# Kernel tuning notes

Measured on AMD Instinct MI355X. Metric: run time of the kernel, lower is better.

Reference implementation:

```python
import jax, jax.numpy as jnp
import numpy as np

N = 50000        # nodes
E = 800000       # edges (before self-loops)
F_IN = 128       # input features
HID = 32         # per-head hidden channels
H1 = 4           # heads of conv1
H2 = 8           # heads of conv2
NEG_SLOPE = 0.2  # PyG GATConv LeakyReLU slope
E_DEC = 100000   # pos/neg decode edges each


def setup_inputs() -> dict:
    key = jax.random.key(0)
    ks = jax.random.split(key, 12)
    s = 0.1
    return {
        "x": jax.random.normal(ks[0], (N, F_IN), jnp.float32),
        "edge_index": jax.random.randint(ks[1], (2, E), 0, N, dtype=jnp.int32),
        "pos_edge_index": jax.random.randint(ks[2], (2, E_DEC), 0, N, dtype=jnp.int32),
        "neg_edge_index": jax.random.randint(ks[3], (2, E_DEC), 0, N, dtype=jnp.int32),
        "W1": jax.random.normal(ks[4], (F_IN, H1 * HID), jnp.float32) * s,
        "a_src1": jax.random.normal(ks[5], (H1, HID), jnp.float32) * s,
        "a_dst1": jax.random.normal(ks[6], (H1, HID), jnp.float32) * s,
        "b1": jax.random.normal(ks[7], (H1 * HID,), jnp.float32) * s,
        "W2": jax.random.normal(ks[8], (H1 * HID, H2 * HID), jnp.float32) * s,
        "a_src2": jax.random.normal(ks[9], (H2, HID), jnp.float32) * s,
        "a_dst2": jax.random.normal(ks[10], (H2, HID), jnp.float32) * s,
        "b2": jax.random.normal(ks[11], (H2 * HID,), jnp.float32) * s,
    }


def _segment_softmax(e, seg, n):
    # softmax over edges grouped by destination node; max is detached (cancels analytically)
    m = jax.lax.stop_gradient(jax.ops.segment_max(e, seg, num_segments=n))
    ex = jnp.exp(e - m[seg])
    denom = jax.ops.segment_sum(ex, seg, num_segments=n)
    return ex / (denom[seg] + 1e-16)


def _gat_conv(x, src, dst, W, a_src, a_dst, b, heads, out_ch):
    n = x.shape[0]
    h = (x @ W).reshape(n, heads, out_ch)             # [N,H,C]
    al_s = (h * a_src[None]).sum(-1)                  # [N,H]
    al_d = (h * a_dst[None]).sum(-1)                  # [N,H]
    e = al_s[src] + al_d[dst]                         # [E,H] edge logits
    e = jnp.where(e > 0, e, NEG_SLOPE * e)            # LeakyReLU
    alpha = _segment_softmax(e, dst, n)               # [E,H]
    msg = h[src] * alpha[:, :, None]                  # [E,H,C]
    out = jax.ops.segment_sum(msg, dst, num_segments=n)  # [N,H,C]
    return out.reshape(n, heads * out_ch) + b


def reference(x, edge_index, pos_edge_index, neg_edge_index,
              W1, a_src1, a_dst1, b1, W2, a_src2, a_dst2, b2):
    n = x.shape[0]
    loops = jnp.arange(n, dtype=edge_index.dtype)     # PyG add_self_loops=True
    src = jnp.concatenate([edge_index[0], loops])
    dst = jnp.concatenate([edge_index[1], loops])
    # encode
    z = jax.nn.relu(_gat_conv(x, src, dst, W1, a_src1, a_dst1, b1, H1, HID))
    z = _gat_conv(z, src, dst, W2, a_src2, a_dst2, b2, H2, HID)
    # decode
    ei = jnp.concatenate([pos_edge_index, neg_edge_index], axis=1)
    logits = (z[ei[0]] * z[ei[1]]).sum(-1)            # [2*E_DEC]
    return logits
```

## Files before the change

### kernel.cpp

```cpp
#include <hip/hip_runtime.h>
#include <hip/hip_bf16.h>

#define NN 50000
#define EE 800000
#define ET (EE + NN)
#define F_IN 128
#define HID 32
#define H1 4
#define H2 8
#define E_DEC 100000
#define NEG_SLOPE 0.2f

typedef __attribute__((ext_vector_type(8))) short short8;
typedef __attribute__((ext_vector_type(4))) float floatx4;

__device__ __forceinline__ unsigned short f2b(float f) {
    __hip_bfloat16 h = __float2bfloat16(f);
    return *reinterpret_cast<unsigned short*>(&h);
}
__device__ __forceinline__ float b2f(unsigned short u) {
    return __uint_as_float(((unsigned int)u) << 16);
}
__device__ __forceinline__ __hip_bfloat162 pack_bf162(float vx, float vy) {
    __hip_bfloat162 o;
    o.x = __float2bfloat16(vx);
    o.y = __float2bfloat16(vy);
    return o;
}

__global__ void fillint_k(int* __restrict__ p, int n) {
    int i = blockIdx.x * blockDim.x + threadIdx.x;
    if (i < n) p[i] = 0;
}

__global__ void hist_k(const int* __restrict__ ei, int* __restrict__ counts) {
    int e = blockIdx.x * blockDim.x + threadIdx.x;
    if (e >= ET) return;
    int d = (e < EE) ? ei[EE + e] : e - EE;
    atomicAdd(&counts[d], 1);
}

__global__ void scan1_k(const int* __restrict__ counts, int* __restrict__ bsum) {
    __shared__ int sh[256];
    int t = threadIdx.x;
    int i = blockIdx.x * 256 + t;
    sh[t] = (i < NN) ? counts[i] : 0;
    __syncthreads();
    for (int off = 128; off > 0; off >>= 1) {
        if (t < off) sh[t] += sh[t + off];
        __syncthreads();
    }
    if (t == 0) bsum[blockIdx.x] = sh[0];
}

__global__ void scan2_k(int* __restrict__ bsum, int nb, int* __restrict__ start) {
    __shared__ int sh[256];
    int t = threadIdx.x;
    int v = (t < nb) ? bsum[t] : 0;
    sh[t] = v;
    __syncthreads();
    for (int off = 1; off < 256; off <<= 1) {
        int u = (t >= off) ? sh[t - off] : 0;
        __syncthreads();
        sh[t] += u;
        __syncthreads();
    }
    if (t < nb) bsum[t] = sh[t] - v;
    if (t == 0) start[NN] = ET;
}

__global__ void scan3_k(const int* __restrict__ counts, const int* __restrict__ bsum,
                        int* __restrict__ start, int* __restrict__ cursor) {
    __shared__ int sh[256];
    int t = threadIdx.x;
    int i = blockIdx.x * 256 + t;
    int c = (i < NN) ? counts[i] : 0;
    sh[t] = c;
    __syncthreads();
    for (int off = 1; off < 256; off <<= 1) {
        int u = (t >= off) ? sh[t - off] : 0;
        __syncthreads();
        sh[t] += u;
        __syncthreads();
    }
    int excl = sh[t] - c + bsum[blockIdx.x];
    if (i < NN) {
        start[i] = excl;
        cursor[i] = excl;
    }
}

__global__ void scatter_k(const int* __restrict__ ei, int* __restrict__ cursor,
                          int* __restrict__ csr) {
    int e = blockIdx.x * blockDim.x + threadIdx.x;
    if (e >= ET) return;
    int s, d;
    if (e < EE) { s = ei[e]; d = ei[EE + e]; } else { s = d = e - EE; }
    int slot = atomicAdd(&cursor[d], 1);
    csr[slot] = s;
}

__global__ void cvt_k(const float4* __restrict__ X, ushort4* __restrict__ Xb, int n4) {
    int i = blockIdx.x * blockDim.x + threadIdx.x;
    if (i >= n4) return;
    float4 v = X[i];
    ushort4 o;
    o.x = f2b(v.x);
    o.y = f2b(v.y);
    o.z = f2b(v.z);
    o.w = f2b(v.w);
    Xb[i] = o;
}

template <int OUT>
__global__ void packW_k(const float* __restrict__ W, unsigned short* __restrict__ Wp) {
    const int total = (OUT / 16) * 4 * 64;
    int id = blockIdx.x * 256 + threadIdx.x;
    if (id >= total) return;
    const int col = ((id >> 8) << 4) + (id & 15);
    const int k0 = ((id >> 6) & 3) * 32 + ((id >> 4) & 3) * 8;
    ushort4 lo, hi;
    lo.x = f2b(W[(k0 + 0) * OUT + col]);
    lo.y = f2b(W[(k0 + 1) * OUT + col]);
    lo.z = f2b(W[(k0 + 2) * OUT + col]);
    lo.w = f2b(W[(k0 + 3) * OUT + col]);
    hi.x = f2b(W[(k0 + 4) * OUT + col]);
    hi.y = f2b(W[(k0 + 5) * OUT + col]);
    hi.z = f2b(W[(k0 + 6) * OUT + col]);
    hi.w = f2b(W[(k0 + 7) * OUT + col]);
    ((ushort4*)Wp)[id * 2] = lo;
    ((ushort4*)Wp)[id * 2 + 1] = hi;
}

template <int OUT, int CT>
__global__ void mfma_gemm_k(const unsigned short* __restrict__ Xb,
                            const unsigned short* __restrict__ Wp,
                            unsigned short* __restrict__ Hout) {
    const int wave = threadIdx.x >> 6;
    const int lane = threadIdx.x & 63;
    const int quad = lane >> 4;
    const int rl = lane & 15;
    const int r0 = blockIdx.x * 64;
    floatx4 acc[4][CT];
#pragma unroll
    for (int rt = 0; rt < 4; ++rt)
#pragma unroll
        for (int ct = 0; ct < CT; ++ct) acc[rt][ct] = {0.f, 0.f, 0.f, 0.f};

#pragma unroll
    for (int ks = 0; ks < 4; ++ks) {
        short8 a[4];
#pragma unroll
        for (int rt = 0; rt < 4; ++rt) {
            int row = r0 + rt * 16 + rl;
            row = row < NN ? row : NN - 1;
            a[rt] = *(const short8*)(Xb + (long long)row * 128 + ks * 32 + quad * 8);
        }
#pragma unroll
        for (int ct = 0; ct < CT; ++ct) {
            const int ctg = wave * CT + ct;
            const short8 b = *(const short8*)(Wp + (((ctg * 4 + ks) * 64 + lane) << 3));
#pragma unroll
            for (int rt = 0; rt < 4; ++rt)
                acc[rt][ct] = __builtin_amdgcn_mfma_f32_16x16x32_bf16(a[rt], b, acc[rt][ct], 0, 0, 0);
        }
    }
#pragma unroll
    for (int rt = 0; rt < 4; ++rt) {
        const int rowbase = r0 + rt * 16 + quad * 4;
#pragma unroll
        for (int ct = 0; ct < CT; ++ct) {
            const int col = (wave * CT + ct) * 16 + rl;
#pragma unroll
            for (int r = 0; r < 4; ++r) {
                const int row = rowbase + r;
                if (row < NN) Hout[(long long)row * OUT + col] = f2b(acc[rt][ct][r]);
            }
        }
    }
}

template <int OUT, int H>
__global__ void al_k(const unsigned short* __restrict__ Hb, const float* __restrict__ a_src,
                     const float* __restrict__ a_dst, float* __restrict__ als,
                     float* __restrict__ ald) {
    const int wave = threadIdx.x >> 6;
    const int lane = threadIdx.x & 63;
    const int row = blockIdx.x * 4 + wave;
    const int CPL = OUT / 64;
    const int G = 32 / CPL;
    const int c0 = lane * CPL;
    const int hd = c0 >> 5;
    float ps = 0.f, pd = 0.f;
#pragma unroll
    for (int j = 0; j < CPL; ++j) {
        const float hv = b2f(Hb[(long long)row * OUT + c0 + j]);
        const int cc = hd * 32 + ((c0 + j) & 31);
        ps += hv * a_src[cc];
        pd += hv * a_dst[cc];
    }
#pragma unroll
    for (int m = G / 2; m >= 1; m >>= 1) {
        ps += __shfl_xor(ps, m, 64);
        pd += __shfl_xor(pd, m, 64);
    }
    if ((lane & (G - 1)) == 0) {
        als[row * H + hd] = ps;
        ald[row * H + hd] = pd;
    }
}

template <int OUT, int H, bool RELU>
__global__ void gather_k(const int* __restrict__ start, const int* __restrict__ csr,
                         const float* __restrict__ als, const float* __restrict__ ald,
                         const __hip_bfloat162* __restrict__ Hin,
                         const float* __restrict__ bias, __hip_bfloat162* __restrict__ outp) {
    const int d = blockIdx.x;
    const int t = threadIdx.x;
    const int hd = t >> 4;
    const int beg = start[d];
    const int end = start[d + 1];
    const float aldd = ald[d * H + hd];
    float accx = 0.f, accy = 0.f, den = 0.f;
    int i = beg;
    for (; i + 4 <= end; i += 4) {
        const int s0 = csr[i], s1 = csr[i + 1], s2 = csr[i + 2], s3 = csr[i + 3];
        float l0 = als[s0 * H + hd] + aldd;
        float l1 = als[s1 * H + hd] + aldd;
        float l2 = als[s2 * H + hd] + aldd;
        float l3 = als[s3 * H + hd] + aldd;
        const __hip_bfloat162 g0 = Hin[(long long)s0 * (OUT / 2) + t];
        const __hip_bfloat162 g1 = Hin[(long long)s1 * (OUT / 2) + t];
        const __hip_bfloat162 g2 = Hin[(long long)s2 * (OUT / 2) + t];
        const __hip_bfloat162 g3 = Hin[(long long)s3 * (OUT / 2) + t];
        l0 = l0 > 0.f ? l0 : NEG_SLOPE * l0;
        l1 = l1 > 0.f ? l1 : NEG_SLOPE * l1;
        l2 = l2 > 0.f ? l2 : NEG_SLOPE * l2;
        l3 = l3 > 0.f ? l3 : NEG_SLOPE * l3;
        const float w0 = __expf(l0), w1 = __expf(l1), w2 = __expf(l2), w3 = __expf(l3);
        den += (w0 + w1) + (w2 + w3);
        const float2 f0 = __bfloat1622float2(g0);
        const float2 f1 = __bfloat1622float2(g1);
        const float2 f2 = __bfloat1622float2(g2);
        const float2 f3 = __bfloat1622float2(g3);
        accx += w0 * f0.x + w1 * f1.x + w2 * f2.x + w3 * f3.x;
        accy += w0 * f0.y + w1 * f1.y + w2 * f2.y + w3 * f3.y;
    }
    for (; i < end; ++i) {
        const int s = csr[i];
        float lg = als[s * H + hd] + aldd;
        lg = lg > 0.f ? lg : NEG_SLOPE * lg;
        const float w = __expf(lg);
        const float2 f = __bfloat1622float2(Hin[(long long)s * (OUT / 2) + t]);
        den += w;
        accx += w * f.x;
        accy += w * f.y;
    }
    const float inv = 1.f / (den + 1e-16f);
    float vx = accx * inv + bias[2 * t];
    float vy = accy * inv + bias[2 * t + 1];
    if (RELU) {
        vx = vx > 0.f ? vx : 0.f;
        vy = vy > 0.f ? vy : 0.f;
    }
    outp[(long long)d * (OUT / 2) + t] = pack_bf162(vx, vy);
}

__global__ void decode_k(const int* __restrict__ pei, const int* __restrict__ nei,
                         const __hip_bfloat162* __restrict__ z2, float* __restrict__ out) {
    const int w = threadIdx.x >> 6, lane = threadIdx.x & 63;
    const int idx = blockIdx.x * 4 + w;
    if (idx >= 2 * E_DEC) return;
    int a, b;
    if (idx < E_DEC) {
        a = pei[idx];
        b = pei[E_DEC + idx];
    } else {
        const int j = idx - E_DEC;
        a = nei[j];
        b = nei[E_DEC + j];
    }
    const __hip_bfloat162* za = z2 + (long long)a * 128;
    const __hip_bfloat162* zb = z2 + (long long)b * 128;
    float s = 0.f;
#pragma unroll
    for (int r = 0; r < 2; ++r) {
        const float2 fa = __bfloat1622float2(za[lane + 64 * r]);
        const float2 fb = __bfloat1622float2(zb[lane + 64 * r]);
        s += fa.x * fb.x + fa.y * fb.y;
    }
#pragma unroll
    for (int m = 32; m >= 1; m >>= 1) s += __shfl_xor(s, m, 64);
    if (lane == 0) out[idx] = s;
}

extern "C" void kernel_launch(void* const* d_in, const int* in_sizes, int n_in,
                              void* d_out, int out_size, void* d_ws, size_t ws_size,
                              hipStream_t stream) {
    const float* x = (const float*)d_in[0];
    const int* ei = (const int*)d_in[1];
    const int* pei = (const int*)d_in[2];
    const int* nei = (const int*)d_in[3];
    const float* W1 = (const float*)d_in[4];
    const float* as1 = (const float*)d_in[5];
    const float* ad1 = (const float*)d_in[6];
    const float* b1 = (const float*)d_in[7];
    const float* W2 = (const float*)d_in[8];
    const float* as2 = (const float*)d_in[9];
    const float* ad2 = (const float*)d_in[10];
    const float* b2 = (const float*)d_in[11];
    float* out = (float*)d_out;

    unsigned short* h1 = (unsigned short*)d_ws;
    unsigned short* h2 = h1 + (long long)NN * 128;
    unsigned short* z2 = h2 + (long long)NN * 256;
    unsigned short* z1 = z2 + (long long)NN * 256;
    unsigned short* xb = z1 + (long long)NN * 128;
    unsigned short* wp1 = xb + (long long)NN * 128;
    unsigned short* wp2 = wp1 + 128 * 128;
    float* als1 = (float*)(wp2 + 128 * 256);
    float* ald1 = als1 + NN * H1;
    float* als2 = ald1 + NN * H1;
    float* ald2 = als2 + NN * H2;
    int* counts = (int*)(ald2 + NN * H2);
    int* start = counts + NN;
    int* cursor = start + NN + 1;
    int* bsum = cursor + NN;
    int* csr = bsum + 256;

    const int NB = (NN + 255) / 256;

    fillint_k<<<NB, 256, 0, stream>>>(counts, NN);
    hist_k<<<(ET + 255) / 256, 256, 0, stream>>>(ei, counts);
    scan1_k<<<NB, 256, 0, stream>>>(counts, bsum);
    scan2_k<<<1, 256, 0, stream>>>(bsum, NB, start);
    scan3_k<<<NB, 256, 0, stream>>>(counts, bsum, start, cursor);
    scatter_k<<<(ET + 255) / 256, 256, 0, stream>>>(ei, cursor, csr);

    const int n4 = NN * 128 / 4;
    cvt_k<<<(n4 + 255) / 256, 256, 0, stream>>>((const float4*)x, (ushort4*)xb, n4);
    packW_k<128><<<(2048 + 255) / 256, 256, 0, stream>>>(W1, wp1);
    packW_k<256><<<(4096 + 255) / 256, 256, 0, stream>>>(W2, wp2);

    mfma_gemm_k<128, 2><<<(NN + 63) / 64, 256, 0, stream>>>(xb, wp1, h1);
    al_k<128, H1><<<NN / 4, 256, 0, stream>>>(h1, as1, ad1, als1, ald1);
    gather_k<128, H1, true><<<NN, 64, 0, stream>>>(
        start, csr, als1, ald1, (const __hip_bfloat162*)h1, b1, (__hip_bfloat162*)z1);

    mfma_gemm_k<256, 4><<<(NN + 63) / 64, 256, 0, stream>>>(z1, wp2, h2);
    al_k<256, H2><<<NN / 4, 256, 0, stream>>>(h2, as2, ad2, als2, ald2);
    gather_k<256, H2, false><<<NN, 128, 0, stream>>>(
        start, csr, als2, ald2, (const __hip_bfloat162*)h2, b2, (__hip_bfloat162*)z2);

    decode_k<<<(2 * E_DEC + 3) / 4, 256, 0, stream>>>(
        pei, nei, (const __hip_bfloat162*)z2, out);
}
```

Measured before the change: 382.2 us.

## Split each node's edge list across waves in GAT gather with shared-memory reduction

The gather kernel now uses 256-thread blocks. Each wave (or half-wave, for the 128-wide layer) handles a strided subset of the destination node's incoming edges and loads 4 bf16 features per lane as one ushort4. Partial sums and denominators are combined by shuffle and then through shared memory before normalisation and bias. This raises the number of edges in flight per node to hide gather latency, at the cost of a __syncthreads and idle threads in the final reduction step. Decode also switches to one 8-byte load per lane.

```diff
diff --git a/kernel.cpp b/kernel.cpp
--- a/kernel.cpp
+++ b/kernel.cpp
@@ -20,12 +20,6 @@
 }
 __device__ __forceinline__ float b2f(unsigned short u) {
     return __uint_as_float(((unsigned int)u) << 16);
-}
-__device__ __forceinline__ __hip_bfloat162 pack_bf162(float vx, float vy) {
-    __hip_bfloat162 o;
-    o.x = __float2bfloat16(vx);
-    o.y = __float2bfloat16(vy);
-    return o;
 }
 
 __global__ void fillint_k(int* __restrict__ p, int n) {
@@ -213,61 +207,83 @@
 template <int OUT, int H, bool RELU>
 __global__ void gather_k(const int* __restrict__ start, const int* __restrict__ csr,
                          const float* __restrict__ als, const float* __restrict__ ald,
-                         const __hip_bfloat162* __restrict__ Hin,
-                         const float* __restrict__ bias, __hip_bfloat162* __restrict__ outp) {
+                         const unsigned short* __restrict__ Hin,
+                         const float* __restrict__ bias, unsigned short* __restrict__ outp) {
+    constexpr int LPR = OUT / 4;
+    constexpr int EPW = 64 / LPR;
+    constexpr int SLOTS = 4 * EPW;
+    constexpr int SHIFT = (EPW == 1) ? 6 : 5;
     const int d = blockIdx.x;
     const int t = threadIdx.x;
-    const int hd = t >> 4;
-    const int beg = start[d];
-    const int end = start[d + 1];
+    const int wave = t >> 6;
+    const int lane = t & 63;
+    const int cl = lane & (LPR - 1);
+    const int slot = wave * EPW + (lane >> SHIFT);
+    const int hd = cl >> 3;
+    const int beg = start[d], end = start[d + 1];
     const float aldd = ald[d * H + hd];
-    float accx = 0.f, accy = 0.f, den = 0.f;
-    int i = beg;
-    for (; i + 4 <= end; i += 4) {
-        const int s0 = csr[i], s1 = csr[i + 1], s2 = csr[i + 2], s3 = csr[i + 3];
-        float l0 = als[s0 * H + hd] + aldd;
-        float l1 = als[s1 * H + hd] + aldd;
-        float l2 = als[s2 * H + hd] + aldd;
-        float l3 = als[s3 * H + hd] + aldd;
-        const __hip_bfloat162 g0 = Hin[(long long)s0 * (OUT / 2) + t];
-        const __hip_bfloat162 g1 = Hin[(long long)s1 * (OUT / 2) + t];
-        const __hip_bfloat162 g2 = Hin[(long long)s2 * (OUT / 2) + t];
-        const __hip_bfloat162 g3 = Hin[(long long)s3 * (OUT / 2) + t];
-        l0 = l0 > 0.f ? l0 : NEG_SLOPE * l0;
-        l1 = l1 > 0.f ? l1 : NEG_SLOPE * l1;
-        l2 = l2 > 0.f ? l2 : NEG_SLOPE * l2;
-        l3 = l3 > 0.f ? l3 : NEG_SLOPE * l3;
-        const float w0 = __expf(l0), w1 = __expf(l1), w2 = __expf(l2), w3 = __expf(l3);
-        den += (w0 + w1) + (w2 + w3);
-        const float2 f0 = __bfloat1622float2(g0);
-        const float2 f1 = __bfloat1622float2(g1);
-        const float2 f2 = __bfloat1622float2(g2);
-        const float2 f3 = __bfloat1622float2(g3);
-        accx += w0 * f0.x + w1 * f1.x + w2 * f2.x + w3 * f3.x;
-        accy += w0 * f0.y + w1 * f1.y + w2 * f2.y + w3 * f3.y;
-    }
-    for (; i < end; ++i) {
+    float a0 = 0.f, a1 = 0.f, a2 = 0.f, a3 = 0.f, den = 0.f;
+    for (int i = beg + slot; i < end; i += SLOTS) {
         const int s = csr[i];
         float lg = als[s * H + hd] + aldd;
         lg = lg > 0.f ? lg : NEG_SLOPE * lg;
         const float w = __expf(lg);
-        const float2 f = __bfloat1622float2(Hin[(long long)s * (OUT / 2) + t]);
+        const ushort4 hv = *(const ushort4*)(Hin + (long long)s * OUT + cl * 4);
         den += w;
-        accx += w * f.x;
-        accy += w * f.y;
-    }
-    const float inv = 1.f / (den + 1e-16f);
-    float vx = accx * inv + bias[2 * t];
-    float vy = accy * inv + bias[2 * t + 1];
-    if (RELU) {
-        vx = vx > 0.f ? vx : 0.f;
-        vy = vy > 0.f ? vy : 0.f;
-    }
-    outp[(long long)d * (OUT / 2) + t] = pack_bf162(vx, vy);
+        a0 += w * b2f(hv.x);
+        a1 += w * b2f(hv.y);
+        a2 += w * b2f(hv.z);
+        a3 += w * b2f(hv.w);
+    }
+    if (EPW == 2) {
+        a0 += __shfl_xor(a0, 32, 64);
+        a1 += __shfl_xor(a1, 32, 64);
+        a2 += __shfl_xor(a2, 32, 64);
+        a3 += __shfl_xor(a3, 32, 64);
+        den += __shfl_xor(den, 32, 64);
+    }
+    __shared__ float sh[4][64][5];
+    if (lane < LPR) {
+        sh[wave][cl][0] = a0;
+        sh[wave][cl][1] = a1;
+        sh[wave][cl][2] = a2;
+        sh[wave][cl][3] = a3;
+        sh[wave][cl][4] = den;
+    }
+    __syncthreads();
+    if (t < LPR) {
+        float s0 = 0.f, s1 = 0.f, s2 = 0.f, s3 = 0.f, dn = 0.f;
+#pragma unroll
+        for (int w = 0; w < 4; ++w) {
+            s0 += sh[w][t][0];
+            s1 += sh[w][t][1];
+            s2 += sh[w][t][2];
+            s3 += sh[w][t][3];
+            dn += sh[w][t][4];
+        }
+        const float inv = 1.f / (dn + 1e-16f);
+        const int c0 = t * 4;
+        float v0 = s0 * inv + bias[c0];
+        float v1 = s1 * inv + bias[c0 + 1];
+        float v2 = s2 * inv + bias[c0 + 2];
+        float v3 = s3 * inv + bias[c0 + 3];
+        if (RELU) {
+            v0 = v0 > 0.f ? v0 : 0.f;
+            v1 = v1 > 0.f ? v1 : 0.f;
+            v2 = v2 > 0.f ? v2 : 0.f;
+            v3 = v3 > 0.f ? v3 : 0.f;
+        }
+        ushort4 o;
+        o.x = f2b(v0);
+        o.y = f2b(v1);
+        o.z = f2b(v2);
+        o.w = f2b(v3);
+        *(ushort4*)(outp + (long long)d * OUT + c0) = o;
+    }
 }
 
 __global__ void decode_k(const int* __restrict__ pei, const int* __restrict__ nei,
-                         const __hip_bfloat162* __restrict__ z2, float* __restrict__ out) {
+                         const unsigned short* __restrict__ z2, float* __restrict__ out) {
     const int w = threadIdx.x >> 6, lane = threadIdx.x & 63;
     const int idx = blockIdx.x * 4 + w;
     if (idx >= 2 * E_DEC) return;
@@ -280,15 +296,10 @@
         a = nei[j];
         b = nei[E_DEC + j];
     }
-    const __hip_bfloat162* za = z2 + (long long)a * 128;
-    const __hip_bfloat162* zb = z2 + (long long)b * 128;
-    float s = 0.f;
-#pragma unroll
-    for (int r = 0; r < 2; ++r) {
-        const float2 fa = __bfloat1622float2(za[lane + 64 * r]);
-        const float2 fb = __bfloat1622float2(zb[lane + 64 * r]);
-        s += fa.x * fb.x + fa.y * fb.y;
-    }
+    const ushort4 ua = *(const ushort4*)(z2 + (long long)a * 256 + lane * 4);
+    const ushort4 ub = *(const ushort4*)(z2 + (long long)b * 256 + lane * 4);
+    float s = b2f(ua.x) * b2f(ub.x) + b2f(ua.y) * b2f(ub.y) +
+              b2f(ua.z) * b2f(ub.z) + b2f(ua.w) * b2f(ub.w);
 #pragma unroll
     for (int m = 32; m >= 1; m >>= 1) s += __shfl_xor(s, m, 64);
     if (lane == 0) out[idx] = s;
@@ -344,14 +355,11 @@
 
     mfma_gemm_k<128, 2><<<(NN + 63) / 64, 256, 0, stream>>>(xb, wp1, h1);
     al_k<128, H1><<<NN / 4, 256, 0, stream>>>(h1, as1, ad1, als1, ald1);
-    gather_k<128, H1, true><<<NN, 64, 0, stream>>>(
-        start, csr, als1, ald1, (const __hip_bfloat162*)h1, b1, (__hip_bfloat162*)z1);
+    gather_k<128, H1, true><<<NN, 256, 0, stream>>>(start, csr, als1, ald1, h1, b1, z1);
 
     mfma_gemm_k<256, 4><<<(NN + 63) / 64, 256, 0, stream>>>(z1, wp2, h2);
     al_k<256, H2><<<NN / 4, 256, 0, stream>>>(h2, as2, ad2, als2, ald2);
-    gather_k<256, H2, false><<<NN, 128, 0, stream>>>(
-        start, csr, als2, ald2, (const __hip_bfloat162*)h2, b2, (__hip_bfloat162*)z2);
-
-    decode_k<<<(2 * E_DEC + 3) / 4, 256, 0, stream>>>(
-        pei, nei, (const __hip_bfloat162*)z2, out);
-}
+    gather_k<256, H2, false><<<NN, 256, 0, stream>>>(start, csr, als2, ald2, h2, b2, z2);
+
+    decode_k<<<(2 * E_DEC + 3) / 4, 256, 0, stream>>>(pei, nei, z2, out);
+}
```

New measurement: 453.4 us. 18.6% more time.
